# Kernel optimization log

Hardware: AMD Instinct MI355X
Metric: run time of the kernel (lower is better)

Reference implementation:

```python
import jax, jax.numpy as jnp
import numpy as np
import math

B, S, E = 8, 128, 192
H = 6
HD = E // H  # 32
L = 64       # latent_dim (hardcoded default in MHLA)
N_EXP = 8
TOP_K = 2
ED = 768     # expert_dim
EPS = 1e-5


def setup_inputs() -> dict:
    key = jax.random.key(0)
    ks = jax.random.split(key, 24)
    sc = 0.02
    nrm = lambda k, shp: (jax.random.normal(k, shp, dtype=jnp.float32) * sc)
    inp = {
        "x": jax.random.normal(ks[0], (B, S, E), dtype=jnp.float32),
        "rms1_w": jnp.ones((E,), jnp.float32),
        "rms2_w": jnp.ones((E,), jnp.float32),
        # latent_tokens: Linear(S*E -> L*E); stored [in, out]
        "latW": nrm(ks[1], (S * E, L * E)),
        "latb": jnp.zeros((L * E,), jnp.float32),
        "qW": nrm(ks[2], (E, E)), "qb": jnp.zeros((E,), jnp.float32),
        "kW": nrm(ks[3], (E, E)), "kb": jnp.zeros((E,), jnp.float32),
        "vW": nrm(ks[4], (E, E)), "vb": jnp.zeros((E,), jnp.float32),
        "oW": nrm(ks[5], (E, E)), "ob": jnp.zeros((E,), jnp.float32),
        "rW": nrm(ks[6], (E, N_EXP)), "rb": jnp.zeros((N_EXP,), jnp.float32),
        # stacked expert params: layer1 (E->ED), swiglu-linear (ED->ED), layer2 (ED->E)
        "e1W": nrm(ks[7], (N_EXP, E, ED)), "e1b": jnp.zeros((N_EXP, ED), jnp.float32),
        "swW": nrm(ks[8], (N_EXP, ED, ED)), "swb": jnp.zeros((N_EXP, ED), jnp.float32),
        "e2W": nrm(ks[9], (N_EXP, ED, E)), "e2b": jnp.zeros((N_EXP, E), jnp.float32),
    }
    return inp


def _rmsnorm(x, w):
    ms = jnp.mean(x * x, axis=-1, keepdims=True)
    return x * jax.lax.rsqrt(ms + EPS) * w


def _rope_q(q):
    # q: [B,H,S,HD]; rotate interleaved pairs, torch-style view(..., HD//2, 2)
    t = jnp.arange(S, dtype=jnp.float32)
    inv_freq = 1.0 / (10000.0 ** (jnp.arange(0, HD, 2, dtype=jnp.float32) / HD))
    freqs = jnp.outer(t, inv_freq)            # [S, HD/2]
    cos, sin = jnp.cos(freqs), jnp.sin(freqs)
    qp = q.reshape(B, H, S, HD // 2, 2)
    x1, x2 = qp[..., 0], qp[..., 1]
    r1 = x1 * cos - x2 * sin
    r2 = x1 * sin + x2 * cos
    return jnp.stack([r1, r2], axis=-1).reshape(B, H, S, HD)


def _mhla(x, latW, latb, qW, qb, kW, kb, vW, vb, oW, ob):
    latent = (x.reshape(B, S * E) @ latW + latb).reshape(B, L, E)
    q = (x @ qW + qb).reshape(B, S, H, HD).transpose(0, 2, 1, 3)       # [B,H,S,HD]
    k = (latent @ kW + kb).reshape(B, L, H, HD).transpose(0, 2, 1, 3)  # [B,H,L,HD]
    v = (latent @ vW + vb).reshape(B, L, H, HD).transpose(0, 2, 1, 3)
    qr = _rope_q(q)  # RoPE applied to query only (key_r = key in source)
    scores = jnp.einsum("bhsd,bhld->bhsl", qr, k) / math.sqrt(HD)
    attn = jax.nn.softmax(scores, axis=-1)
    out = jnp.einsum("bhsl,bhld->bhsd", attn, v)
    out = out.transpose(0, 2, 1, 3).reshape(B, S, E)
    return out @ oW + ob


def _moe(h, rW, rb, e1W, e1b, swW, swb, e2W, e2b):
    probs = jax.nn.softmax(h @ rW + rb, axis=-1)          # [B,S,N]
    pk, idx = jax.lax.top_k(probs, TOP_K)                 # [B,S,K]
    # dense all-expert compute (8 small experts), then gather top-k
    t1 = jnp.einsum("bse,neh->bsnh", h, e1W) + e1b        # [B,S,N,ED]
    t2 = jax.nn.relu(jnp.einsum("bsnh,nhg->bsng", t1, swW) + swb)
    eo = jnp.einsum("bsng,nge->bsne", t2, e2W) + e2b      # [B,S,N,E]
    sel = jnp.take_along_axis(eo, idx[..., None], axis=2) # [B,S,K,E]
    return jnp.sum(pk[..., None] * sel, axis=2)


def reference(x, rms1_w, rms2_w, latW, latb, qW, qb, kW, kb, vW, vb, oW, ob,
              rW, rb, e1W, e1b, swW, swb, e2W, e2b):
    x = x + _mhla(_rmsnorm(x, rms1_w), latW, latb, qW, qb, kW, kb, vW, vb, oW, ob)
    x = x + _moe(_rmsnorm(x, rms2_w), rW, rb, e1W, e1b, swW, swb, e2W, e2b)
    return x
```

## Files before the change

kernel.cpp:

```cpp
#include <hip/hip_runtime.h>
#include <hip/hip_bf16.h>
#include <math.h>

#define B 8
#define S 128
#define E 192
#define H 6
#define HD 32
#define L 64
#define NEXP 8
#define ED 768
#define T (B*S)
#define SE (S*E)
#define LE (L*E)

#define SPLITS 64
#define ISPAN 384
#define CHUNK 128

using s8 = __attribute__((ext_vector_type(8))) short;
using f4 = __attribute__((ext_vector_type(4))) float;

__global__ __launch_bounds__(64) void rmsnorm_bf_k(const float* __restrict__ x,
                                                   const float* __restrict__ w,
                                                   float* __restrict__ y,
                                                   __hip_bfloat16* __restrict__ yb) {
  int row = blockIdx.x;
  int lane = threadIdx.x;
  const float* xr = x + (size_t)row * E;
  float v0 = xr[lane], v1 = xr[lane + 64], v2 = xr[lane + 128];
  float s = v0 * v0 + v1 * v1 + v2 * v2;
#pragma unroll
  for (int off = 32; off > 0; off >>= 1) s += __shfl_xor(s, off);
  float inv = rsqrtf(s * (1.0f / E) + 1e-5f);
  float r0 = v0 * inv * w[lane];
  float r1 = v1 * inv * w[lane + 64];
  float r2 = v2 * inv * w[lane + 128];
  float* yr = y + (size_t)row * E;
  __hip_bfloat16* yrb = yb + (size_t)row * E;
  yr[lane] = r0; yr[lane + 64] = r1; yr[lane + 128] = r2;
  yrb[lane] = __float2bfloat16(r0);
  yrb[lane + 64] = __float2bfloat16(r1);
  yrb[lane + 128] = __float2bfloat16(r2);
}

__global__ __launch_bounds__(256) void lat_partial_k(const float* __restrict__ xn,
                                                     const float* __restrict__ latW,
                                                     float* __restrict__ part) {
  const int tid = threadIdx.x;
  const int j = blockIdx.x * 1024 + tid * 4;
  const int i0 = blockIdx.y * ISPAN;
  __shared__ float xs[CHUNK][8];
  f4 acc[8];
#pragma unroll
  for (int b = 0; b < 8; ++b) acc[b] = (f4){0.f, 0.f, 0.f, 0.f};
  for (int c = 0; c < ISPAN; c += CHUNK) {
    float* xsf = (float*)xs;
    __syncthreads();
    for (int l = tid; l < CHUNK * 8; l += 256) {
      int ii = l >> 3, b = l & 7;
      xsf[l] = xn[(size_t)b * SE + i0 + c + ii];
    }
    __syncthreads();
#pragma unroll 8
    for (int ii = 0; ii < CHUNK; ++ii) {
      const f4 w = __builtin_nontemporal_load(
          (const f4*)&latW[(size_t)(i0 + c + ii) * LE + j]);
#pragma unroll
      for (int b = 0; b < 8; ++b) {
        float xv = xs[ii][b];
        acc[b][0] += xv * w[0];
        acc[b][1] += xv * w[1];
        acc[b][2] += xv * w[2];
        acc[b][3] += xv * w[3];
      }
    }
  }
#pragma unroll
  for (int b = 0; b < 8; ++b)
    *(f4*)&part[((size_t)blockIdx.y * 8 + b) * LE + j] = acc[b];
}

__global__ __launch_bounds__(256) void lat_reduce_k(const float* __restrict__ part,
                                                    const float* __restrict__ latb,
                                                    __hip_bfloat16* __restrict__ lat16) {
  int g = blockIdx.x * 256 + threadIdx.x;
  int b = g / LE, j = g - b * LE;
  float s = latb[j];
  for (int sp = 0; sp < SPLITS; ++sp) s += part[((size_t)sp * 8 + b) * LE + j];
  lat16[g] = __float2bfloat16(s);
}

__global__ __launch_bounds__(256) void tconv4_k(const float* __restrict__ qW,
                                                const float* __restrict__ kW,
                                                const float* __restrict__ vW,
                                                const float* __restrict__ oW,
                                                __hip_bfloat16* __restrict__ qWt,
                                                __hip_bfloat16* __restrict__ kWt,
                                                __hip_bfloat16* __restrict__ vWt,
                                                __hip_bfloat16* __restrict__ oWt) {
  const int z = blockIdx.z;
  const float* in = (z == 0) ? qW : (z == 1) ? kW : (z == 2) ? vW : oW;
  __hip_bfloat16* out = (z == 0) ? qWt : (z == 1) ? kWt : (z == 2) ? vWt : oWt;
  __shared__ float tile[32][33];
  int tx = threadIdx.x & 31, r8 = threadIdx.x >> 5;
  int k0 = blockIdx.x * 32, n0 = blockIdx.y * 32;
#pragma unroll
  for (int i = 0; i < 4; ++i)
    tile[r8 + 8 * i][tx] = in[(size_t)(k0 + r8 + 8 * i) * E + n0 + tx];
  __syncthreads();
#pragma unroll
  for (int i = 0; i < 4; ++i) {
    int nr = r8 + 8 * i;
    out[(size_t)(n0 + nr) * E + k0 + tx] = __float2bfloat16(tile[tx][nr]);
  }
}

__global__ __launch_bounds__(256) void tconv_k(const float* __restrict__ in,
                                               __hip_bfloat16* __restrict__ out,
                                               int K, int N) {
  const int e = blockIdx.z;
  in += (size_t)e * K * N;
  out += (size_t)e * N * K;
  __shared__ float tile[32][33];
  int tx = threadIdx.x & 31, r8 = threadIdx.x >> 5;
  int k0 = blockIdx.x * 32, n0 = blockIdx.y * 32;
#pragma unroll
  for (int i = 0; i < 4; ++i)
    tile[r8 + 8 * i][tx] = in[(size_t)(k0 + r8 + 8 * i) * N + n0 + tx];
  __syncthreads();
#pragma unroll
  for (int i = 0; i < 4; ++i) {
    int nr = r8 + 8 * i;
    out[(size_t)(n0 + nr) * K + k0 + tx] = __float2bfloat16(tile[tx][nr]);
  }
}

__global__ __launch_bounds__(256) void qkv_mm_k(const __hip_bfloat16* __restrict__ xnb,
                                                const __hip_bfloat16* __restrict__ lat16,
                                                const __hip_bfloat16* __restrict__ qWt,
                                                const __hip_bfloat16* __restrict__ kWt,
                                                const __hip_bfloat16* __restrict__ vWt,
                                                const float* __restrict__ qb,
                                                const float* __restrict__ kb,
                                                const float* __restrict__ vb,
                                                float* __restrict__ qo,
                                                float* __restrict__ ko,
                                                float* __restrict__ vo) {
  const int z = blockIdx.z;
  const int M = (z == 0) ? T : (B * L);
  const int m0 = blockIdx.y * 128;
  if (m0 >= M) return;
  const short* A = (const short*)((z == 0) ? xnb : lat16);
  const short* Wt = (const short*)((z == 0) ? qWt : (z == 1) ? kWt : vWt);
  const float* bias = (z == 0) ? qb : (z == 1) ? kb : vb;
  float* C = (z == 0) ? qo : (z == 1) ? ko : vo;
  const int n0 = blockIdx.x * 64;
  __shared__ short As[128 * 64];
  __shared__ short Bs[64 * 64];
  const int tid = threadIdx.x;
  const int lane = tid & 63, wid = tid >> 6;
  const int wr = wid >> 1, wc = wid & 1;
  const int lr = lane & 15, lg = lane >> 4;
  const int slot = tid & 7;
  f4 acc[4][2];
#pragma unroll
  for (int fm = 0; fm < 4; ++fm)
#pragma unroll
    for (int fn = 0; fn < 2; ++fn) acc[fm][fn] = (f4){0.f, 0.f, 0.f, 0.f};
  for (int kb2 = 0; kb2 < E; kb2 += 64) {
    __syncthreads();
#pragma unroll
    for (int p = 0; p < 4; ++p) {
      int row = p * 32 + (tid >> 3);
      s8 v = *(const s8*)(A + (size_t)(m0 + row) * E + kb2 + slot * 8);
      *(s8*)&As[row * 64 + ((slot ^ (row & 7)) << 3)] = v;
    }
#pragma unroll
    for (int p = 0; p < 2; ++p) {
      int row = p * 32 + (tid >> 3);
      s8 v = *(const s8*)(Wt + (size_t)(n0 + row) * E + kb2 + slot * 8);
      *(s8*)&Bs[row * 64 + ((slot ^ (row & 7)) << 3)] = v;
    }
    __syncthreads();
#pragma unroll
    for (int kk = 0; kk < 64; kk += 32) {
      const int sb = (kk >> 3) + lg;
      s8 af[4], bf[2];
#pragma unroll
      for (int fm = 0; fm < 4; ++fm) {
        int row = wr * 64 + fm * 16 + lr;
        af[fm] = *(const s8*)&As[row * 64 + ((sb ^ (row & 7)) << 3)];
      }
#pragma unroll
      for (int fn = 0; fn < 2; ++fn) {
        int row = wc * 32 + fn * 16 + lr;
        bf[fn] = *(const s8*)&Bs[row * 64 + ((sb ^ (row & 7)) << 3)];
      }
#pragma unroll
      for (int fm = 0; fm < 4; ++fm)
#pragma unroll
        for (int fn = 0; fn < 2; ++fn)
          acc[fm][fn] = __builtin_amdgcn_mfma_f32_16x16x32_bf16(af[fm], bf[fn], acc[fm][fn], 0, 0, 0);
    }
  }
#pragma unroll
  for (int fm = 0; fm < 4; ++fm)
#pragma unroll
    for (int fn = 0; fn < 2; ++fn) {
      int col = n0 + wc * 32 + fn * 16 + lr;
      int rowb = m0 + wr * 64 + fm * 16 + lg * 4;
      float bv = bias[col];
#pragma unroll
      for (int j = 0; j < 4; ++j)
        C[(size_t)(rowb + j) * E + col] = acc[fm][fn][j] + bv;
    }
}

__global__ __launch_bounds__(256) void oproj_mm_k(const __hip_bfloat16* __restrict__ aob,
                                                  const __hip_bfloat16* __restrict__ oWt,
                                                  const float* __restrict__ ob,
                                                  const float* __restrict__ x,
                                                  float* __restrict__ x1) {
  const int m0 = blockIdx.y * 128;
  const int n0 = blockIdx.x * 64;
  const short* A = (const short*)aob;
  const short* Wt = (const short*)oWt;
  __shared__ short As[128 * 64];
  __shared__ short Bs[64 * 64];
  const int tid = threadIdx.x;
  const int lane = tid & 63, wid = tid >> 6;
  const int wr = wid >> 1, wc = wid & 1;
  const int lr = lane & 15, lg = lane >> 4;
  const int slot = tid & 7;
  f4 acc[4][2];
#pragma unroll
  for (int fm = 0; fm < 4; ++fm)
#pragma unroll
    for (int fn = 0; fn < 2; ++fn) acc[fm][fn] = (f4){0.f, 0.f, 0.f, 0.f};
  for (int kb2 = 0; kb2 < E; kb2 += 64) {
    __syncthreads();
#pragma unroll
    for (int p = 0; p < 4; ++p) {
      int row = p * 32 + (tid >> 3);
      s8 v = *(const s8*)(A + (size_t)(m0 + row) * E + kb2 + slot * 8);
      *(s8*)&As[row * 64 + ((slot ^ (row & 7)) << 3)] = v;
    }
#pragma unroll
    for (int p = 0; p < 2; ++p) {
      int row = p * 32 + (tid >> 3);
      s8 v = *(const s8*)(Wt + (size_t)(n0 + row) * E + kb2 + slot * 8);
      *(s8*)&Bs[row * 64 + ((slot ^ (row & 7)) << 3)] = v;
    }
    __syncthreads();
#pragma unroll
    for (int kk = 0; kk < 64; kk += 32) {
      const int sb = (kk >> 3) + lg;
      s8 af[4], bf[2];
#pragma unroll
      for (int fm = 0; fm < 4; ++fm) {
        int row = wr * 64 + fm * 16 + lr;
        af[fm] = *(const s8*)&As[row * 64 + ((sb ^ (row & 7)) << 3)];
      }
#pragma unroll
      for (int fn = 0; fn < 2; ++fn) {
        int row = wc * 32 + fn * 16 + lr;
        bf[fn] = *(const s8*)&Bs[row * 64 + ((sb ^ (row & 7)) << 3)];
      }
#pragma unroll
      for (int fm = 0; fm < 4; ++fm)
#pragma unroll
        for (int fn = 0; fn < 2; ++fn)
          acc[fm][fn] = __builtin_amdgcn_mfma_f32_16x16x32_bf16(af[fm], bf[fn], acc[fm][fn], 0, 0, 0);
    }
  }
#pragma unroll
  for (int fm = 0; fm < 4; ++fm)
#pragma unroll
    for (int fn = 0; fn < 2; ++fn) {
      int col = n0 + wc * 32 + fn * 16 + lr;
      int rowb = m0 + wr * 64 + fm * 16 + lg * 4;
      float bv = ob[col];
#pragma unroll
      for (int j = 0; j < 4; ++j) {
        size_t off = (size_t)(rowb + j) * E + col;
        x1[off] = acc[fm][fn][j] + bv + x[off];
      }
    }
}

__global__ __launch_bounds__(64) void router_rms_k(const float* __restrict__ x1,
                                                   const float* __restrict__ w,
                                                   const float* __restrict__ rW,
                                                   const float* __restrict__ rb,
                                                   __hip_bfloat16* __restrict__ hb,
                                                   float* __restrict__ pk,
                                                   int* __restrict__ idx) {
  int t = blockIdx.x;
  int lane = threadIdx.x;
  const float* xr = x1 + (size_t)t * E;
  float v0 = xr[lane], v1 = xr[lane + 64], v2 = xr[lane + 128];
  float s = v0 * v0 + v1 * v1 + v2 * v2;
#pragma unroll
  for (int off = 32; off > 0; off >>= 1) s += __shfl_xor(s, off);
  float inv = rsqrtf(s * (1.0f / E) + 1e-5f);
  float r0 = v0 * inv * w[lane];
  float r1 = v1 * inv * w[lane + 64];
  float r2 = v2 * inv * w[lane + 128];
  __hip_bfloat16* yrb = hb + (size_t)t * E;
  yrb[lane] = __float2bfloat16(r0);
  yrb[lane + 64] = __float2bfloat16(r1);
  yrb[lane + 128] = __float2bfloat16(r2);
  float lg[8];
#pragma unroll
  for (int n = 0; n < 8; ++n)
    lg[n] = r0 * rW[lane * 8 + n] + r1 * rW[(lane + 64) * 8 + n] + r2 * rW[(lane + 128) * 8 + n];
#pragma unroll
  for (int n = 0; n < 8; ++n)
#pragma unroll
    for (int off = 32; off > 0; off >>= 1) lg[n] += __shfl_xor(lg[n], off);
  if (lane == 0) {
#pragma unroll
    for (int n = 0; n < 8; ++n) lg[n] += rb[n];
    float mx = lg[0];
#pragma unroll
    for (int n = 1; n < 8; ++n) mx = fmaxf(mx, lg[n]);
    float p[8], sum = 0.f;
#pragma unroll
    for (int n = 0; n < 8; ++n) { p[n] = __expf(lg[n] - mx); sum += p[n]; }
    float isum = 1.f / sum;
#pragma unroll
    for (int n = 0; n < 8; ++n) p[n] *= isum;
    int i0 = 0;
#pragma unroll
    for (int n = 1; n < 8; ++n) if (p[n] > p[i0]) i0 = n;
    int i1 = (i0 == 0) ? 1 : 0;
#pragma unroll
    for (int n = 0; n < 8; ++n) if (n != i0 && p[n] > p[i1]) i1 = n;
    pk[t * 2] = p[i0];
    pk[t * 2 + 1] = p[i1];
    idx[t * 2] = i0;
    idx[t * 2 + 1] = i1;
  }
}

__global__ __launch_bounds__(512) void compact_k(const int* __restrict__ idx,
                                                 int* __restrict__ toklist,
                                                 int* __restrict__ ppos,
                                                 int* __restrict__ cnt) {
  int e = threadIdx.x >> 6;
  int lane = threadIdx.x & 63;
  int pos = 0;
  for (int base = 0; base < T; base += 64) {
    int t = base + lane;
    int i0 = idx[t * 2], i1 = idx[t * 2 + 1];
    bool sel = (i0 == e) || (i1 == e);
    unsigned long long m = __ballot(sel);
    int myoff = __popcll(m & ((1ull << lane) - 1ull));
    if (sel) {
      int p = pos + myoff;
      toklist[e * T + p] = t;
      ppos[t * 2 + ((i0 == e) ? 0 : 1)] = p;
    }
    pos += __popcll(m);
  }
  if (lane == 0) cnt[e] = pos;
}

__global__ __launch_bounds__(256) void moe_gemm_g(const __hip_bfloat16* __restrict__ A_,
                                                  const __hip_bfloat16* __restrict__ Wt_,
                                                  const float* __restrict__ bias_,
                                                  void* __restrict__ C_,
                                                  const int* __restrict__ toklist,
                                                  const int* __restrict__ cntp,
                                                  int N, int K,
                                                  long aB, long wB, long bB, long cB,
                                                  int flags) {
  const int e = blockIdx.z;
  const int cnt = cntp[e];
  const int m0 = blockIdx.y * 128;
  if (m0 >= cnt) return;
  const short* A = (const short*)A_ + ((flags & 4) ? 0 : (size_t)e * aB);
  const short* Wt = (const short*)Wt_ + (size_t)e * wB;
  const float* bias = bias_ + (size_t)e * bB;
  const int n0 = blockIdx.x * 64;
  __shared__ short As[128 * 64];
  __shared__ short Bs[64 * 64];
  const int tid = threadIdx.x;
  const int lane = tid & 63, wid = tid >> 6;
  const int wr = wid >> 1, wc = wid & 1;
  const int lr = lane & 15, lg = lane >> 4;
  long arow_off[4];
#pragma unroll
  for (int p = 0; p < 4; ++p) {
    int row = p * 32 + (tid >> 3);
    int gr = m0 + row;
    int src;
    if (flags & 4) src = (gr < cnt) ? toklist[e * T + gr] : toklist[e * T];
    else src = gr;
    arow_off[p] = (size_t)src * K;
  }
  f4 acc[4][2];
#pragma unroll
  for (int fm = 0; fm < 4; ++fm)
#pragma unroll
    for (int fn = 0; fn < 2; ++fn) acc[fm][fn] = (f4){0.f, 0.f, 0.f, 0.f};
  const int slot = tid & 7;
  for (int kb = 0; kb < K; kb += 64) {
    __syncthreads();
#pragma unroll
    for (int p = 0; p < 4; ++p) {
      int row = p * 32 + (tid >> 3);
      s8 v = *(const s8*)(A + arow_off[p] + kb + slot * 8);
      *(s8*)&As[row * 64 + ((slot ^ (row & 7)) << 3)] = v;
    }
#pragma unroll
    for (int p = 0; p < 2; ++p) {
      int row = p * 32 + (tid >> 3);
      s8 v = *(const s8*)(Wt + (size_t)(n0 + row) * K + kb + slot * 8);
      *(s8*)&Bs[row * 64 + ((slot ^ (row & 7)) << 3)] = v;
    }
    __syncthreads();
#pragma unroll
    for (int kk = 0; kk < 64; kk += 32) {
      const int sb = (kk >> 3) + lg;
      s8 af[4], bf[2];
#pragma unroll
      for (int fm = 0; fm < 4; ++fm) {
        int row = wr * 64 + fm * 16 + lr;
        af[fm] = *(const s8*)&As[row * 64 + ((sb ^ (row & 7)) << 3)];
      }
#pragma unroll
      for (int fn = 0; fn < 2; ++fn) {
        int row = wc * 32 + fn * 16 + lr;
        bf[fn] = *(const s8*)&Bs[row * 64 + ((sb ^ (row & 7)) << 3)];
      }
#pragma unroll
      for (int fm = 0; fm < 4; ++fm)
#pragma unroll
        for (int fn = 0; fn < 2; ++fn)
          acc[fm][fn] = __builtin_amdgcn_mfma_f32_16x16x32_bf16(af[fm], bf[fn], acc[fm][fn], 0, 0, 0);
    }
  }
#pragma unroll
  for (int fm = 0; fm < 4; ++fm) {
#pragma unroll
    for (int fn = 0; fn < 2; ++fn) {
      int col = n0 + wc * 32 + fn * 16 + lr;
      int rowb = m0 + wr * 64 + fm * 16 + lg * 4;
      float bv = bias[col];
#pragma unroll
      for (int j = 0; j < 4; ++j) {
        if (rowb + j >= cnt) continue;
        float v = acc[fm][fn][j] + bv;
        if (flags & 1) v = fmaxf(v, 0.f);
        if (flags & 2)
          ((float*)C_)[(size_t)e * cB + (size_t)(rowb + j) * N + col] = v;
        else
          ((__hip_bfloat16*)C_)[(size_t)e * cB + (size_t)(rowb + j) * N + col] = __float2bfloat16(v);
      }
    }
  }
}

__global__ __launch_bounds__(128) void attn_k(const float* __restrict__ q,
                                              const float* __restrict__ kk,
                                              const float* __restrict__ vv,
                                              __hip_bfloat16* __restrict__ aob) {
  int b = blockIdx.x / H, h = blockIdx.x % H;
  __shared__ float ks[64][32], vs[64][32];
  int tid = threadIdx.x;
  {
    int l = tid >> 1, hf = (tid & 1) * 16;
    const float4* ksrc = (const float4*)&kk[(size_t)(b * L + l) * E + h * HD + hf];
    const float4* vsrc = (const float4*)&vv[(size_t)(b * L + l) * E + h * HD + hf];
    float4* kdst = (float4*)&ks[l][hf];
    float4* vdst = (float4*)&vs[l][hf];
#pragma unroll
    for (int u = 0; u < 4; ++u) { kdst[u] = ksrc[u]; vdst[u] = vsrc[u]; }
  }
  __syncthreads();
  int s = tid;
  const float* qp = &q[(size_t)(b * S + s) * E + h * HD];
  float qv[32];
#pragma unroll
  for (int d = 0; d < 32; ++d) qv[d] = qp[d];
#pragma unroll
  for (int d = 0; d < 16; ++d) {
    float invf = exp2f(-(float)d * (13.287712379549449f / 16.0f));
    float ang = (float)s * invf;
    float sn, cs;
    __sincosf(ang, &sn, &cs);
    float x1 = qv[2 * d], x2 = qv[2 * d + 1];
    qv[2 * d] = x1 * cs - x2 * sn;
    qv[2 * d + 1] = x1 * sn + x2 * cs;
  }
  const float scale = 0.17677669529663687f;
  float mx = -1e30f;
  for (int l = 0; l < 64; ++l) {
    float dot = 0.f;
#pragma unroll
    for (int d = 0; d < 32; ++d) dot += qv[d] * ks[l][d];
    mx = fmaxf(mx, dot * scale);
  }
  float o[32];
#pragma unroll
  for (int d = 0; d < 32; ++d) o[d] = 0.f;
  float sum = 0.f;
  for (int l = 0; l < 64; ++l) {
    float dot = 0.f;
#pragma unroll
    for (int d = 0; d < 32; ++d) dot += qv[d] * ks[l][d];
    float wgt = __expf(dot * scale - mx);
    sum += wgt;
#pragma unroll
    for (int d = 0; d < 32; ++d) o[d] += wgt * vs[l][d];
  }
  float inv = 1.0f / sum;
  __hip_bfloat16* op = &aob[(size_t)(b * S + s) * E + h * HD];
#pragma unroll
  for (int d = 0; d < 32; ++d) op[d] = __float2bfloat16(o[d] * inv);
}

__global__ __launch_bounds__(256) void combine_k(const float* __restrict__ x1,
                                                 const float* __restrict__ eoc,
                                                 const float* __restrict__ pk,
                                                 const int* __restrict__ idx,
                                                 const int* __restrict__ ppos,
                                                 float* __restrict__ out) {
  int g = blockIdx.x * 256 + threadIdx.x;
  int t = g / E;
  int e = g - t * E;
  int i0 = idx[t * 2], i1 = idx[t * 2 + 1];
  int p0 = ppos[t * 2], p1 = ppos[t * 2 + 1];
  out[g] = x1[g] + pk[t * 2] * eoc[((size_t)i0 * T + p0) * E + e]
                 + pk[t * 2 + 1] * eoc[((size_t)i1 * T + p1) * E + e];
}

extern "C" void kernel_launch(void* const* d_in, const int* in_sizes, int n_in,
                              void* d_out, int out_size, void* d_ws, size_t ws_size,
                              hipStream_t stream) {
  const float* x    = (const float*)d_in[0];
  const float* r1w  = (const float*)d_in[1];
  const float* r2w  = (const float*)d_in[2];
  const float* latW = (const float*)d_in[3];
  const float* latb = (const float*)d_in[4];
  const float* qW   = (const float*)d_in[5];
  const float* qb   = (const float*)d_in[6];
  const float* kW   = (const float*)d_in[7];
  const float* kb   = (const float*)d_in[8];
  const float* vW   = (const float*)d_in[9];
  const float* vb   = (const float*)d_in[10];
  const float* oW   = (const float*)d_in[11];
  const float* ob   = (const float*)d_in[12];
  const float* rW   = (const float*)d_in[13];
  const float* rb   = (const float*)d_in[14];
  const float* e1W  = (const float*)d_in[15];
  const float* e1b  = (const float*)d_in[16];
  const float* swW  = (const float*)d_in[17];
  const float* swb  = (const float*)d_in[18];
  const float* e2W  = (const float*)d_in[19];
  const float* e2b  = (const float*)d_in[20];
  float* out = (float*)d_out;

  float* ws = (float*)d_ws;
  float* xn1  = ws;
  __hip_bfloat16* xnb   = (__hip_bfloat16*)(ws + 196608);
  __hip_bfloat16* lat16 = (__hip_bfloat16*)(ws + 294912);
  float* qbuf = ws + 344064;
  float* kbuf = ws + 540672;
  float* vbuf = ws + 638976;
  __hip_bfloat16* aob   = (__hip_bfloat16*)(ws + 737280);
  float* x1   = ws + 835584;
  float* pk   = ws + 1032192;
  int*   idx  = (int*)(ws + 1034240);
  int*   toklist = (int*)(ws + 1036288);
  int*   ppos    = (int*)(ws + 1044480);
  int*   cnt     = (int*)(ws + 1046528);
  __hip_bfloat16* qWt = (__hip_bfloat16*)(ws + 1046784);
  __hip_bfloat16* kWt = (__hip_bfloat16*)(ws + 1065216);
  __hip_bfloat16* vWt = (__hip_bfloat16*)(ws + 1083648);
  __hip_bfloat16* oWt = (__hip_bfloat16*)(ws + 1102080);
  __hip_bfloat16* hb    = (__hip_bfloat16*)(ws + 1120512);
  __hip_bfloat16* e1Wt  = (__hip_bfloat16*)(ws + 1218816);
  __hip_bfloat16* swWt  = (__hip_bfloat16*)(ws + 1808640);
  __hip_bfloat16* e2Wt  = (__hip_bfloat16*)(ws + 4167936);
  __hip_bfloat16* t1    = (__hip_bfloat16*)(ws + 4757760);
  __hip_bfloat16* t2    = (__hip_bfloat16*)(ws + 7903488);
  float* eoc  = ws + 11049216;
  float* part = ws + 12622080;

  tconv_k<<<dim3(E / 32, ED / 32, NEXP), 256, 0, stream>>>(e1W, e1Wt, E, ED);
  tconv_k<<<dim3(ED / 32, ED / 32, NEXP), 256, 0, stream>>>(swW, swWt, ED, ED);
  tconv_k<<<dim3(ED / 32, E / 32, NEXP), 256, 0, stream>>>(e2W, e2Wt, ED, E);
  tconv4_k<<<dim3(6, 6, 4), 256, 0, stream>>>(qW, kW, vW, oW, qWt, kWt, vWt, oWt);

  rmsnorm_bf_k<<<T, 64, 0, stream>>>(x, r1w, xn1, xnb);
  lat_partial_k<<<dim3(12, SPLITS), 256, 0, stream>>>(xn1, latW, part);
  lat_reduce_k<<<(8 * LE) / 256, 256, 0, stream>>>(part, latb, lat16);
  qkv_mm_k<<<dim3(3, 8, 3), 256, 0, stream>>>(xnb, lat16, qWt, kWt, vWt,
                                              qb, kb, vb, qbuf, kbuf, vbuf);
  attn_k<<<B * H, 128, 0, stream>>>(qbuf, kbuf, vbuf, aob);
  oproj_mm_k<<<dim3(3, 8), 256, 0, stream>>>(aob, oWt, ob, x, x1);
  router_rms_k<<<T, 64, 0, stream>>>(x1, r2w, rW, rb, hb, pk, idx);
  compact_k<<<1, 512, 0, stream>>>(idx, toklist, ppos, cnt);
  moe_gemm_g<<<dim3(ED / 64, 8, NEXP), 256, 0, stream>>>(
      hb, e1Wt, e1b, t1, toklist, cnt, ED, E, 0, (long)ED * E, ED, (long)T * ED, 4);
  moe_gemm_g<<<dim3(ED / 64, 8, NEXP), 256, 0, stream>>>(
      t1, swWt, swb, t2, toklist, cnt, ED, ED, (long)T * ED, (long)ED * ED, ED, (long)T * ED, 1);
  moe_gemm_g<<<dim3(E / 64, 8, NEXP), 256, 0, stream>>>(
      t2, e2Wt, e2b, eoc, toklist, cnt, E, ED, (long)T * ED, (long)E * ED, E, (long)T * E, 2);
  combine_k<<<(T * E) / 256, 256, 0, stream>>>(x1, eoc, pk, idx, ppos, out);
}
```

Measured before the change: 322.3 us.

## Fuse weight transposes into latent GEMV kernel and split attention rows across threads

Result: faster. 303.4 us, median of 2 (-5.9%).

```diff
diff --git a/kernel.cpp b/kernel.cpp
--- a/kernel.cpp
+++ b/kernel.cpp
@@ -44,41 +44,101 @@
   yrb[lane + 128] = __float2bfloat16(r2);
 }
 
-__global__ __launch_bounds__(256) void lat_partial_k(const float* __restrict__ xn,
-                                                     const float* __restrict__ latW,
-                                                     float* __restrict__ part) {
+__global__ __launch_bounds__(256) void mega_k(const float* __restrict__ xn,
+                                              const float* __restrict__ latW,
+                                              float* __restrict__ part,
+                                              const float* __restrict__ e1W,
+                                              const float* __restrict__ swW,
+                                              const float* __restrict__ e2W,
+                                              const float* __restrict__ qW,
+                                              const float* __restrict__ kW,
+                                              const float* __restrict__ vW,
+                                              const float* __restrict__ oW,
+                                              __hip_bfloat16* __restrict__ e1Wt,
+                                              __hip_bfloat16* __restrict__ swWt,
+                                              __hip_bfloat16* __restrict__ e2Wt,
+                                              __hip_bfloat16* __restrict__ qWt,
+                                              __hip_bfloat16* __restrict__ kWt,
+                                              __hip_bfloat16* __restrict__ vWt,
+                                              __hip_bfloat16* __restrict__ oWt) {
+  __shared__ float smem[1056];
+  const int bid = blockIdx.x;
   const int tid = threadIdx.x;
-  const int j = blockIdx.x * 1024 + tid * 4;
-  const int i0 = blockIdx.y * ISPAN;
-  __shared__ float xs[CHUNK][8];
-  f4 acc[8];
-#pragma unroll
-  for (int b = 0; b < 8; ++b) acc[b] = (f4){0.f, 0.f, 0.f, 0.f};
-  for (int c = 0; c < ISPAN; c += CHUNK) {
-    float* xsf = (float*)xs;
+  if (bid < 768) {
+    const int jb = bid % 12, sp = bid / 12;
+    const int j = jb * 1024 + tid * 4;
+    const int i0 = sp * ISPAN;
+    float (*xs)[8] = (float(*)[8])smem;
+    f4 acc[8];
+#pragma unroll
+    for (int b = 0; b < 8; ++b) acc[b] = (f4){0.f, 0.f, 0.f, 0.f};
+    for (int c = 0; c < ISPAN; c += CHUNK) {
+      __syncthreads();
+      for (int l = tid; l < CHUNK * 8; l += 256) {
+        int ii = l >> 3, b = l & 7;
+        smem[l] = xn[(size_t)b * SE + i0 + c + ii];
+      }
+      __syncthreads();
+#pragma unroll 8
+      for (int ii = 0; ii < CHUNK; ++ii) {
+        const f4 w = __builtin_nontemporal_load(
+            (const f4*)&latW[(size_t)(i0 + c + ii) * LE + j]);
+#pragma unroll
+        for (int b = 0; b < 8; ++b) {
+          float xv = xs[ii][b];
+          acc[b][0] += xv * w[0];
+          acc[b][1] += xv * w[1];
+          acc[b][2] += xv * w[2];
+          acc[b][3] += xv * w[3];
+        }
+      }
+    }
+#pragma unroll
+    for (int b = 0; b < 8; ++b)
+      *(f4*)&part[((size_t)sp * 8 + b) * LE + j] = acc[b];
+  } else {
+    int t = bid - 768;
+    const float* in;
+    __hip_bfloat16* outp;
+    int K, N, kb, nb;
+    if (t < 1152) {
+      int e = t / 144, r = t % 144;
+      kb = r % 6; nb = r / 6;
+      in = e1W + (size_t)e * E * ED; outp = e1Wt + (size_t)e * E * ED;
+      K = E; N = ED;
+    } else if (t < 1152 + 4608) {
+      int t2 = t - 1152;
+      int e = t2 / 576, r = t2 % 576;
+      kb = r % 24; nb = r / 24;
+      in = swW + (size_t)e * ED * ED; outp = swWt + (size_t)e * ED * ED;
+      K = ED; N = ED;
+    } else if (t < 1152 + 4608 + 1152) {
+      int t3 = t - 5760;
+      int e = t3 / 144, r = t3 % 144;
+      kb = r % 24; nb = r / 24;
+      in = e2W + (size_t)e * ED * E; outp = e2Wt + (size_t)e * ED * E;
+      K = ED; N = E;
+    } else {
+      int t4 = t - 6912;
+      int z = t4 / 36, r = t4 % 36;
+      kb = r % 6; nb = r / 6;
+      in = (z == 0) ? qW : (z == 1) ? kW : (z == 2) ? vW : oW;
+      outp = (z == 0) ? qWt : (z == 1) ? kWt : (z == 2) ? vWt : oWt;
+      K = E; N = E;
+    }
+    float (*tile)[33] = (float(*)[33])smem;
+    int tx = tid & 31, r8 = tid >> 5;
+    int k0 = kb * 32, n0 = nb * 32;
+#pragma unroll
+    for (int i = 0; i < 4; ++i)
+      tile[r8 + 8 * i][tx] = in[(size_t)(k0 + r8 + 8 * i) * N + n0 + tx];
     __syncthreads();
-    for (int l = tid; l < CHUNK * 8; l += 256) {
-      int ii = l >> 3, b = l & 7;
-      xsf[l] = xn[(size_t)b * SE + i0 + c + ii];
-    }
-    __syncthreads();
-#pragma unroll 8
-    for (int ii = 0; ii < CHUNK; ++ii) {
-      const f4 w = __builtin_nontemporal_load(
-          (const f4*)&latW[(size_t)(i0 + c + ii) * LE + j]);
-#pragma unroll
-      for (int b = 0; b < 8; ++b) {
-        float xv = xs[ii][b];
-        acc[b][0] += xv * w[0];
-        acc[b][1] += xv * w[1];
-        acc[b][2] += xv * w[2];
-        acc[b][3] += xv * w[3];
-      }
-    }
-  }
-#pragma unroll
-  for (int b = 0; b < 8; ++b)
-    *(f4*)&part[((size_t)blockIdx.y * 8 + b) * LE + j] = acc[b];
+#pragma unroll
+    for (int i = 0; i < 4; ++i) {
+      int nr = r8 + 8 * i;
+      outp[(size_t)(n0 + nr) * K + k0 + tx] = __float2bfloat16(tile[tx][nr]);
+    }
+  }
 }
 
 __global__ __launch_bounds__(256) void lat_reduce_k(const float* __restrict__ part,
@@ -89,51 +149,6 @@
   float s = latb[j];
   for (int sp = 0; sp < SPLITS; ++sp) s += part[((size_t)sp * 8 + b) * LE + j];
   lat16[g] = __float2bfloat16(s);
-}
-
-__global__ __launch_bounds__(256) void tconv4_k(const float* __restrict__ qW,
-                                                const float* __restrict__ kW,
-                                                const float* __restrict__ vW,
-                                                const float* __restrict__ oW,
-                                                __hip_bfloat16* __restrict__ qWt,
-                                                __hip_bfloat16* __restrict__ kWt,
-                                                __hip_bfloat16* __restrict__ vWt,
-                                                __hip_bfloat16* __restrict__ oWt) {
-  const int z = blockIdx.z;
-  const float* in = (z == 0) ? qW : (z == 1) ? kW : (z == 2) ? vW : oW;
-  __hip_bfloat16* out = (z == 0) ? qWt : (z == 1) ? kWt : (z == 2) ? vWt : oWt;
-  __shared__ float tile[32][33];
-  int tx = threadIdx.x & 31, r8 = threadIdx.x >> 5;
-  int k0 = blockIdx.x * 32, n0 = blockIdx.y * 32;
-#pragma unroll
-  for (int i = 0; i < 4; ++i)
-    tile[r8 + 8 * i][tx] = in[(size_t)(k0 + r8 + 8 * i) * E + n0 + tx];
-  __syncthreads();
-#pragma unroll
-  for (int i = 0; i < 4; ++i) {
-    int nr = r8 + 8 * i;
-    out[(size_t)(n0 + nr) * E + k0 + tx] = __float2bfloat16(tile[tx][nr]);
-  }
-}
-
-__global__ __launch_bounds__(256) void tconv_k(const float* __restrict__ in,
-                                               __hip_bfloat16* __restrict__ out,
-                                               int K, int N) {
-  const int e = blockIdx.z;
-  in += (size_t)e * K * N;
-  out += (size_t)e * N * K;
-  __shared__ float tile[32][33];
-  int tx = threadIdx.x & 31, r8 = threadIdx.x >> 5;
-  int k0 = blockIdx.x * 32, n0 = blockIdx.y * 32;
-#pragma unroll
-  for (int i = 0; i < 4; ++i)
-    tile[r8 + 8 * i][tx] = in[(size_t)(k0 + r8 + 8 * i) * N + n0 + tx];
-  __syncthreads();
-#pragma unroll
-  for (int i = 0; i < 4; ++i) {
-    int nr = r8 + 8 * i;
-    out[(size_t)(n0 + nr) * K + k0 + tx] = __float2bfloat16(tile[tx][nr]);
-  }
 }
 
 __global__ __launch_bounds__(256) void qkv_mm_k(const __hip_bfloat16* __restrict__ xnb,
@@ -463,63 +478,69 @@
   }
 }
 
-__global__ __launch_bounds__(128) void attn_k(const float* __restrict__ q,
+__global__ __launch_bounds__(256) void attn_k(const float* __restrict__ q,
                                               const float* __restrict__ kk,
                                               const float* __restrict__ vv,
                                               __hip_bfloat16* __restrict__ aob) {
   int b = blockIdx.x / H, h = blockIdx.x % H;
   __shared__ float ks[64][32], vs[64][32];
-  int tid = threadIdx.x;
-  {
-    int l = tid >> 1, hf = (tid & 1) * 16;
-    const float4* ksrc = (const float4*)&kk[(size_t)(b * L + l) * E + h * HD + hf];
-    const float4* vsrc = (const float4*)&vv[(size_t)(b * L + l) * E + h * HD + hf];
-    float4* kdst = (float4*)&ks[l][hf];
-    float4* vdst = (float4*)&vs[l][hf];
-#pragma unroll
-    for (int u = 0; u < 4; ++u) { kdst[u] = ksrc[u]; vdst[u] = vsrc[u]; }
+  __shared__ float sc[64][128];
+  const int tid = threadIdx.x;
+#pragma unroll
+  for (int i = 0; i < 2; ++i) {
+    int fi = tid + 256 * i;
+    int l = fi >> 3, c = (fi & 7) << 2;
+    *(float4*)&ks[l][c] = *(const float4*)&kk[(size_t)(b * L + l) * E + h * HD + c];
+    *(float4*)&vs[l][c] = *(const float4*)&vv[(size_t)(b * L + l) * E + h * HD + c];
   }
   __syncthreads();
-  int s = tid;
-  const float* qp = &q[(size_t)(b * S + s) * E + h * HD];
-  float qv[32];
-#pragma unroll
-  for (int d = 0; d < 32; ++d) qv[d] = qp[d];
-#pragma unroll
-  for (int d = 0; d < 16; ++d) {
-    float invf = exp2f(-(float)d * (13.287712379549449f / 16.0f));
-    float ang = (float)s * invf;
+  const int qrow = tid >> 1, half = tid & 1;
+  const float* qp = &q[(size_t)(b * S + qrow) * E + h * HD + half * 16];
+  float qv[16];
+#pragma unroll
+  for (int d = 0; d < 16; ++d) qv[d] = qp[d];
+  const float TBL[16] = {
+    1.0f, 0.5623413251903491f, 0.31622776601683794f, 0.17782794100389228f,
+    0.1f, 0.05623413251903491f, 0.031622776601683794f, 0.017782794100389228f,
+    0.01f, 0.005623413251903491f, 0.0031622776601683794f, 0.0017782794100389228f,
+    0.001f, 0.0005623413251903491f, 0.00031622776601683794f, 0.00017782794100389228f};
+#pragma unroll
+  for (int dd = 0; dd < 8; ++dd) {
+    float ang = (float)qrow * TBL[half * 8 + dd];
     float sn, cs;
     __sincosf(ang, &sn, &cs);
-    float x1 = qv[2 * d], x2 = qv[2 * d + 1];
-    qv[2 * d] = x1 * cs - x2 * sn;
-    qv[2 * d + 1] = x1 * sn + x2 * cs;
+    float x1 = qv[2 * dd], x2 = qv[2 * dd + 1];
+    qv[2 * dd] = x1 * cs - x2 * sn;
+    qv[2 * dd + 1] = x1 * sn + x2 * cs;
   }
   const float scale = 0.17677669529663687f;
+#pragma unroll
+  for (int d = 0; d < 16; ++d) qv[d] *= scale;
+  const int cbase = half * 16;
   float mx = -1e30f;
   for (int l = 0; l < 64; ++l) {
-    float dot = 0.f;
-#pragma unroll
-    for (int d = 0; d < 32; ++d) dot += qv[d] * ks[l][d];
-    mx = fmaxf(mx, dot * scale);
-  }
-  float o[32];
-#pragma unroll
-  for (int d = 0; d < 32; ++d) o[d] = 0.f;
+    float p = 0.f;
+#pragma unroll
+    for (int d = 0; d < 16; ++d) p += qv[d] * ks[l][cbase + d];
+    p += __shfl_xor(p, 1);
+    if (!half) sc[l][qrow] = p;
+    mx = fmaxf(mx, p);
+  }
+  __syncthreads();
+  float o[16];
+#pragma unroll
+  for (int d = 0; d < 16; ++d) o[d] = 0.f;
   float sum = 0.f;
   for (int l = 0; l < 64; ++l) {
-    float dot = 0.f;
-#pragma unroll
-    for (int d = 0; d < 32; ++d) dot += qv[d] * ks[l][d];
-    float wgt = __expf(dot * scale - mx);
+    float wgt = __expf(sc[l][qrow] - mx);
     sum += wgt;
 #pragma unroll
-    for (int d = 0; d < 32; ++d) o[d] += wgt * vs[l][d];
+    for (int d = 0; d < 16; ++d) o[d] += wgt * vs[l][cbase + d];
   }
   float inv = 1.0f / sum;
-  __hip_bfloat16* op = &aob[(size_t)(b * S + s) * E + h * HD];
-#pragma unroll
-  for (int d = 0; d < 32; ++d) op[d] = __float2bfloat16(o[d] * inv);
+  __hip_bfloat16* op = &aob[(size_t)(b * S + qrow) * E + h * HD + cbase];
+#pragma unroll
+  for (int d = 0; d < 16; ++d) op[d] = __float2bfloat16(o[d] * inv);
 }
 
 __global__ __launch_bounds__(256) void combine_k(const float* __restrict__ x1,
@@ -590,17 +611,14 @@
   float* eoc  = ws + 11049216;
   float* part = ws + 12622080;
 
-  tconv_k<<<dim3(E / 32, ED / 32, NEXP), 256, 0, stream>>>(e1W, e1Wt, E, ED);
-  tconv_k<<<dim3(ED / 32, ED / 32, NEXP), 256, 0, stream>>>(swW, swWt, ED, ED);
-  tconv_k<<<dim3(ED / 32, E / 32, NEXP), 256, 0, stream>>>(e2W, e2Wt, ED, E);
-  tconv4_k<<<dim3(6, 6, 4), 256, 0, stream>>>(qW, kW, vW, oW, qWt, kWt, vWt, oWt);
-
   rmsnorm_bf_k<<<T, 64, 0, stream>>>(x, r1w, xn1, xnb);
-  lat_partial_k<<<dim3(12, SPLITS), 256, 0, stream>>>(xn1, latW, part);
+  mega_k<<<7824, 256, 0, stream>>>(xn1, latW, part,
+                                   e1W, swW, e2W, qW, kW, vW, oW,
+                                   e1Wt, swWt, e2Wt, qWt, kWt, vWt, oWt);
   lat_reduce_k<<<(8 * LE) / 256, 256, 0, stream>>>(part, latb, lat16);
   qkv_mm_k<<<dim3(3, 8, 3), 256, 0, stream>>>(xnb, lat16, qWt, kWt, vWt,
                                               qb, kb, vb, qbuf, kbuf, vbuf);
-  attn_k<<<B * H, 128, 0, stream>>>(qbuf, kbuf, vbuf, aob);
+  attn_k<<<B * H, 256, 0, stream>>>(qbuf, kbuf, vbuf, aob);
   oproj_mm_k<<<dim3(3, 8), 256, 0, stream>>>(aob, oWt, ob, x, x1);
   router_rms_k<<<T, 64, 0, stream>>>(x1, r2w, rW, rb, hb, pk, idx);
   compact_k<<<1, 512, 0, stream>>>(idx, toklist, ppos, cnt);
```
